# Kernel tuning notes

Measured on AMD Instinct MI355X. Metric: run time of the kernel, lower is better.

The kernel has to match this reference:

```python
import jax, jax.numpy as jnp
import numpy as np

B, C, W = 8, 128, 4096
REDUCTION = 8
D = C // REDUCTION  # 16


def setup_inputs() -> dict:
    key = jax.random.key(0)
    ks = jax.random.split(key, 7)
    scale = 0.05
    return {
        "x": jax.random.normal(ks[0], (B, C, W), dtype=jnp.float32),
        "Wq": jax.random.normal(ks[1], (D, C), dtype=jnp.float32) * scale,
        "bq": jax.random.normal(ks[2], (D,), dtype=jnp.float32) * scale,
        "Wk": jax.random.normal(ks[3], (D, C), dtype=jnp.float32) * scale,
        "bk": jax.random.normal(ks[4], (D,), dtype=jnp.float32) * scale,
        "Wv": jax.random.normal(ks[5], (C, C), dtype=jnp.float32) * scale,
        "bv": jax.random.normal(ks[6], (C,), dtype=jnp.float32) * scale,
    }


def reference(x, Wq, bq, Wk, bk, Wv, bv):
    # 1x1 Conv1d == per-position linear over channel axis
    q = jnp.einsum('dc,bcw->bdw', Wq, x) + bq[None, :, None]   # [B, D, W]
    k = jnp.einsum('dc,bcw->bdw', Wk, x) + bk[None, :, None]   # [B, D, W]
    v = jnp.einsum('oc,bcw->bow', Wv, x) + bv[None, :, None]   # [B, C, W]
    scale = D ** (-0.5)
    # scores[b,i,j] = q[b,:,i] . k[b,:,j]
    scores = jnp.einsum('bdi,bdj->bij', q, k) * scale          # [B, W, W]
    attn = jax.nn.softmax(scores, axis=-1)
    # torch.bmm(value, attn): context[b,c,w] = sum_j v[b,c,j] * attn[b,j,w]
    context = jnp.einsum('bcj,bjw->bcw', v, attn)              # [B, C, W]
    return context + x
```

## Files before the change

kernel.cpp:

```cpp
#include <hip/hip_runtime.h>

#define B_ 8
#define C_ 128
#define W_ 4096
#define D_ 16
#define SCALE2 0.3606737602222409f

typedef short bf16x8 __attribute__((ext_vector_type(8)));
typedef float f32x4 __attribute__((ext_vector_type(4)));
typedef float f32x16 __attribute__((ext_vector_type(16)));

__device__ __forceinline__ unsigned short f2bf(float f) {
    unsigned int u = __float_as_uint(f);
    u += 0x7fffu + ((u >> 16) & 1u);
    return (unsigned short)(u >> 16);
}
__device__ __forceinline__ float bf2f(unsigned short h) {
    return __uint_as_float(((unsigned int)h) << 16);
}
__device__ __forceinline__ unsigned int pk2bf(float lo, float hi) {
    return __builtin_amdgcn_perm(__float_as_uint(hi), __float_as_uint(lo), 0x07060302u);
}
__device__ __forceinline__ bf16x8 u4_to_bf8(unsigned int a, unsigned int b,
                                            unsigned int c, unsigned int d) {
    union { uint4 u; bf16x8 v; } t;
    t.u = make_uint4(a, b, c, d);
    return t.v;
}
__device__ __forceinline__ bf16x8 uint4_as_bf8(uint4 u) {
    union { uint4 u; bf16x8 v; } t;
    t.u = u;
    return t.v;
}
__device__ __forceinline__ uint4 exp2pkq(f32x16 s, int r0) {
    return make_uint4(
        pk2bf(__builtin_amdgcn_exp2f(s[r0+0]), __builtin_amdgcn_exp2f(s[r0+1])),
        pk2bf(__builtin_amdgcn_exp2f(s[r0+2]), __builtin_amdgcn_exp2f(s[r0+3])),
        pk2bf(__builtin_amdgcn_exp2f(s[r0+4]), __builtin_amdgcn_exp2f(s[r0+5])),
        pk2bf(__builtin_amdgcn_exp2f(s[r0+6]), __builtin_amdgcn_exp2f(s[r0+7])));
}
__device__ __forceinline__ int xswz(int j, int c8) {
    return c8 ^ (j & 7) ^ ((j >> 3) & 7);
}

__global__ __launch_bounds__(256) void prep(
    const float* __restrict__ Wq, const float* __restrict__ Wk, const float* __restrict__ Wv,
    unsigned short* __restrict__ Wvbf, unsigned short* __restrict__ Wqkbf)
{
    int g = blockIdx.x * 256 + threadIdx.x;
    const float* src; unsigned short* dst; float sc = 1.0f;
    if (g < 4096)      { src = Wv + g * 4;            dst = Wvbf + g * 4; }
    else if (g < 4608) { int t = g - 4096; src = Wq + t * 4; dst = Wqkbf + t * 4; sc = SCALE2; }
    else               { int t = g - 4608; src = Wk + t * 4; dst = Wqkbf + 2048 + t * 4; }
    float4 v = *(const float4*)src;
    unsigned short h[4] = {f2bf(v.x * sc), f2bf(v.y * sc), f2bf(v.z * sc), f2bf(v.w * sc)};
    *(ushort4*)dst = *(ushort4*)h;
}

__global__ __launch_bounds__(256) void proj(
    const float* __restrict__ x, const unsigned short* __restrict__ Wvbf,
    const unsigned short* __restrict__ Wqkbf,
    const float* __restrict__ bqp, const float* __restrict__ bkp, const float* __restrict__ bvp,
    unsigned short* __restrict__ qws2, unsigned short* __restrict__ kws2,
    unsigned short* __restrict__ vws2)
{
    __shared__ unsigned short xbf[32 * 128];
    __shared__ unsigned short outs[128 * 36];
    __shared__ unsigned short qk_s[2][32][24];

    int b  = blockIdx.x & 7;
    int j0 = (blockIdx.x >> 3) * 32;
    int jt = j0 >> 5;
    int tid = threadIdx.x;
    int wid = tid >> 6, lane = tid & 63, n = lane & 15, q4 = lane >> 4;

    {
        unsigned int* xbf32 = (unsigned int*)xbf;
#pragma unroll
        for (int i = 0; i < 8; i++) {
            int p = tid + 256 * i;
            int c2 = p >> 5;
            int j  = p & 31;
            const float* xp = x + (size_t)(b * C_ + 2 * c2) * W_ + j0 + j;
            float lo = xp[0];
            float hi = xp[W_];
            xbf32[j * 64 + xswz(j, c2 >> 2) * 4 + (c2 & 3)] = pk2bf(lo, hi);
        }
    }
    __syncthreads();

    const f32x4 zero = {0.f, 0.f, 0.f, 0.f};
    f32x4 accv[2][2]; f32x4 accqk = zero;
#pragma unroll
    for (int os = 0; os < 2; os++)
#pragma unroll
        for (int js = 0; js < 2; js++) accv[os][js] = zero;

    int isK = wid >> 1;
    int jsm = wid & 1;

#pragma unroll
    for (int kk = 0; kk < 128; kk += 32) {
        bf16x8 av[2], aqkf, bx[2];
#pragma unroll
        for (int os = 0; os < 2; os++)
            av[os] = *(const bf16x8*)(Wvbf + (wid * 32 + os * 16 + n) * 128 + kk + q4 * 8);
        aqkf = *(const bf16x8*)(Wqkbf + (isK * 16 + n) * 128 + kk + q4 * 8);
#pragma unroll
        for (int js = 0; js < 2; js++) {
            int j = js * 16 + n;
            bx[js] = *(const bf16x8*)&xbf[j * 128 + xswz(j, (kk >> 3) + q4) * 8];
        }
#pragma unroll
        for (int os = 0; os < 2; os++)
#pragma unroll
            for (int js = 0; js < 2; js++)
                accv[os][js] = __builtin_amdgcn_mfma_f32_16x16x32_bf16(av[os], bx[js], accv[os][js], 0, 0, 0);
        accqk = __builtin_amdgcn_mfma_f32_16x16x32_bf16(aqkf, bx[jsm], accqk, 0, 0, 0);
    }

    {
        int pos = jsm * 16 + n;
        const float* bias = isK ? bkp : bqp;
        float bsc = isK ? 1.0f : SCALE2;
#pragma unroll
        for (int r = 0; r < 4; r++)
            qk_s[isK][pos][q4 * 4 + r] = f2bf(accqk[r] + bias[q4 * 4 + r] * bsc);
    }

    float bvv[2][4];
#pragma unroll
    for (int os = 0; os < 2; os++)
#pragma unroll
        for (int r = 0; r < 4; r++) bvv[os][r] = bvp[wid * 32 + os * 16 + q4 * 4 + r];
#pragma unroll
    for (int os = 0; os < 2; os++)
#pragma unroll
        for (int js = 0; js < 2; js++)
#pragma unroll
            for (int r = 0; r < 4; r++) {
                int c = wid * 32 + os * 16 + q4 * 4 + r;
                int j = js * 16 + n;
                outs[c * 36 + j] = f2bf(accv[os][js][r] + bvv[os][r]);
            }
    __syncthreads();

    if (tid < 128) {
        int qk = tid >> 6, hh = (tid >> 5) & 1, jl = tid & 31;
        uint4 v = *(const uint4*)&qk_s[qk][jl][hh * 8];
        unsigned short* dst = (qk ? kws2 : qws2)
            + (size_t)(b * 128 + jt) * 512 + hh * 256 + jl * 8;
        *(uint4*)dst = v;
    }
#pragma unroll
    for (int rep = 0; rep < 2; rep++) {
        int t = tid + rep * 256;
        int c = t & 127, sel = t >> 7;
        int jb = (sel >> 1) * 16 + (sel & 1) * 4;
        uint2 lo = *(const uint2*)&outs[c * 36 + jb];
        uint2 hi = *(const uint2*)&outs[c * 36 + jb + 8];
        *(uint4*)(vws2 + ((size_t)(b * 128 + jt) * 4 + sel) * 1024 + c * 8) =
            make_uint4(lo.x, lo.y, hi.x, hi.y);
    }
}

__global__ __launch_bounds__(256) void row_stats(
    const unsigned short* __restrict__ qws2, const unsigned short* __restrict__ kws2,
    float* __restrict__ rlp)
{
    int blk = blockIdx.x;
    int b = blk & 7;
    int j0 = ((blk >> 3) & 31) * 128;
    int wsp = blk >> 8;
    int tid = threadIdx.x;
    int wid = tid >> 6, lane = tid & 63, wl = lane & 31, h = lane >> 5;

    const unsigned short* qb = qws2 + (size_t)b * 65536;
    const unsigned short* kb = kws2 + (size_t)b * 65536;
    int jt = (j0 >> 5) + wid;

    bf16x8 aq = *(const bf16x8*)(qb + (size_t)jt * 512 + h * 256 + wl * 8);
    f32x16 zero16 = {0.f,0.f,0.f,0.f,0.f,0.f,0.f,0.f,0.f,0.f,0.f,0.f,0.f,0.f,0.f,0.f};

    float lt[16];
#pragma unroll
    for (int r = 0; r < 16; r++) lt[r] = 0.f;

    bf16x8 bkc = *(const bf16x8*)(kb + (size_t)(wsp * 32) * 512 + h * 256 + wl * 8);
    for (int t = 0; t < 32; t++) {
        f32x16 s = __builtin_amdgcn_mfma_f32_32x32x16_bf16(aq, bkc, zero16, 0, 0, 0);
        int tn = wsp * 32 + ((t + 1) & 31);
        bkc = *(const bf16x8*)(kb + (size_t)tn * 512 + h * 256 + wl * 8);
#pragma unroll
        for (int r = 0; r < 16; r++) lt[r] += __builtin_amdgcn_exp2f(s[r]);
    }
#pragma unroll
    for (int mask = 1; mask < 32; mask <<= 1)
#pragma unroll
        for (int r = 0; r < 16; r++) lt[r] += __shfl_xor(lt[r], mask, 64);
    if (wl == 0) {
#pragma unroll
        for (int g = 0; g < 4; g++) {
            f32x4 v = {lt[4*g+0], lt[4*g+1], lt[4*g+2], lt[4*g+3]};
            *(f32x4*)(rlp + (size_t)wsp * 32768 + (size_t)b * W_ + j0 + wid * 32 + 4 * h + 8 * g) = v;
        }
    }
}

__global__ __launch_bounds__(256) void finl(const float* __restrict__ rlp,
                                            float* __restrict__ rls)
{
    int g = blockIdx.x * 256 + threadIdx.x;
    float l = rlp[g] + rlp[32768 + g] + rlp[65536 + g] + rlp[98304 + g];
    rls[g] = 1.0f / l;
}

__global__ __launch_bounds__(256) void vscale(unsigned short* __restrict__ vws2,
                                              const float* __restrict__ rls)
{
    int g = blockIdx.x * 256 + threadIdx.x;
    int hh = (g >> 7) & 1, kf = (g >> 8) & 1, jt = (g >> 9) & 127, b = g >> 16;
    int jb = jt * 32 + kf * 16 + 4 * hh;
    const float* rp = rls + (size_t)b * W_ + jb;
    float4 r0 = *(const float4*)rp;
    float4 r1 = *(const float4*)(rp + 8);
    uint4 v = *(const uint4*)(vws2 + (size_t)g * 8);
    unsigned int o0 = pk2bf(bf2f((unsigned short)(v.x & 0xffffu)) * r0.x,
                            bf2f((unsigned short)(v.x >> 16))     * r0.y);
    unsigned int o1 = pk2bf(bf2f((unsigned short)(v.y & 0xffffu)) * r0.z,
                            bf2f((unsigned short)(v.y >> 16))     * r0.w);
    unsigned int o2 = pk2bf(bf2f((unsigned short)(v.z & 0xffffu)) * r1.x,
                            bf2f((unsigned short)(v.z >> 16))     * r1.y);
    unsigned int o3 = pk2bf(bf2f((unsigned short)(v.w & 0xffffu)) * r1.z,
                            bf2f((unsigned short)(v.w >> 16))     * r1.w);
    *(uint4*)(vws2 + (size_t)g * 8) = make_uint4(o0, o1, o2, o3);
}

__global__ __launch_bounds__(512, 4) void attn_out(
    const float* __restrict__ x, const unsigned short* __restrict__ qws2,
    const unsigned short* __restrict__ kws2, const unsigned short* __restrict__ vws2,
    float* __restrict__ out)
{
    __shared__ uint4 p_lds[2][1024];
    __shared__ float red[128 * 68];

    int b  = blockIdx.x & 7;
    int w0 = (blockIdx.x >> 3) * 64;
    int tid = threadIdx.x;
    int wid = tid >> 6, lane = tid & 63, wl = lane & 31, h = lane >> 5;
    int cq = wid >> 1, kh = wid & 1;

    const unsigned short* qb  = qws2 + (size_t)b * 65536;
    const unsigned short* kb  = kws2 + (size_t)b * 65536;
    const uint4* vtb4 = (const uint4*)(vws2 + (size_t)b * 524288) + h * 128 + (cq * 32 + wl);
    const int qoff = h * 256 + wl * 8;

    bf16x8 bk = *(const bf16x8*)(kb + (size_t)((w0 >> 5) + kh) * 512 + h * 256 + wl * 8);

    f32x16 zero16 = {0.f,0.f,0.f,0.f,0.f,0.f,0.f,0.f,0.f,0.f,0.f,0.f,0.f,0.f,0.f,0.f};
    f32x16 acc[2];
    acc[0] = zero16; acc[1] = zero16;

    const int wbase = cq * 256 + h * 64 + kh * 32 + wl;
    const int rbase = kh * 512 + h * 64 + wl;

    bf16x8 aq = *(const bf16x8*)(qb + (size_t)cq * 512 + qoff);
    uint4 vf[4];
#pragma unroll
    for (int kf = 0; kf < 4; kf++)
        vf[kf] = vtb4[(size_t)(kh * 4 + kf) * 256];
    {
        f32x16 s = __builtin_amdgcn_mfma_f32_32x32x16_bf16(aq, bk, zero16, 0, 0, 0);
        aq = *(const bf16x8*)(qb + (size_t)(4 + cq) * 512 + qoff);
        p_lds[0][wbase]       = exp2pkq(s, 0);
        p_lds[0][wbase + 128] = exp2pkq(s, 8);
    }
    __syncthreads();

#pragma unroll 2
    for (int it = 0; it < 32; it++) {
        int cur = it & 1, nxt = cur ^ 1;
        uint4 vfn[4];
#pragma unroll
        for (int kf = 0; kf < 4; kf++) {
            int kg = ((it + 1) & 31) * 8 + kh * 4 + kf;
            vfn[kf] = vtb4[(size_t)kg * 256];
        }
        f32x16 s = __builtin_amdgcn_mfma_f32_32x32x16_bf16(aq, bk, zero16, 0, 0, 0);
        aq = *(const bf16x8*)(qb + (size_t)(((it + 2) & 31) * 4 + cq) * 512 + qoff);
        p_lds[nxt][wbase]       = exp2pkq(s, 0);
        p_lds[nxt][wbase + 128] = exp2pkq(s, 8);
        __builtin_amdgcn_s_setprio(1);
#pragma unroll
        for (int kf = 0; kf < 4; kf++) {
            bf16x8 af = uint4_as_bf8(vf[kf]);
#pragma unroll
            for (int nt = 0; nt < 2; nt++) {
                bf16x8 bp = uint4_as_bf8(p_lds[cur][rbase + kf * 128 + nt * 32]);
                acc[nt] = __builtin_amdgcn_mfma_f32_32x32x16_bf16(af, bp, acc[nt], 0, 0, 0);
            }
        }
        __builtin_amdgcn_s_setprio(0);
        __syncthreads();
#pragma unroll
        for (int kf = 0; kf < 4; kf++) vf[kf] = vfn[kf];
    }

#define CROW(r) (cq * 32 + ((r) & 3) + 8 * ((r) >> 2) + 4 * h)
    if (kh == 1) {
#pragma unroll
        for (int nt = 0; nt < 2; nt++)
#pragma unroll
            for (int r = 0; r < 16; r++)
                red[CROW(r) * 68 + nt * 32 + wl] = acc[nt][r];
    }
    __syncthreads();
    if (kh == 0) {
#pragma unroll
        for (int nt = 0; nt < 2; nt++)
#pragma unroll
            for (int r = 0; r < 16; r++) {
                int o = CROW(r) * 68 + nt * 32 + wl;
                red[o] += acc[nt][r];
            }
    }
#undef CROW
    __syncthreads();

#pragma unroll
    for (int u = 0; u < 4; u++) {
        int k = tid + 512 * u;
        int c = k >> 4, wseg = (k & 15) * 4;
        size_t gidx = (size_t)(b * C_ + c) * W_ + w0 + wseg;
        float4 xv = *(const float4*)(x + gidx);
        const float* sp = &red[c * 68 + wseg];
        *(float4*)(out + gidx) = make_float4(sp[0] + xv.x, sp[1] + xv.y, sp[2] + xv.z, sp[3] + xv.w);
    }
}

extern "C" void kernel_launch(void* const* d_in, const int* in_sizes, int n_in,
                              void* d_out, int out_size, void* d_ws, size_t ws_size,
                              hipStream_t stream)
{
    const float* x  = (const float*)d_in[0];
    const float* Wq = (const float*)d_in[1];
    const float* bq = (const float*)d_in[2];
    const float* Wk = (const float*)d_in[3];
    const float* bk = (const float*)d_in[4];
    const float* Wv = (const float*)d_in[5];
    const float* bv = (const float*)d_in[6];
    float* out = (float*)d_out;

    unsigned short* qws2 = (unsigned short*)d_ws;
    unsigned short* kws2 = qws2 + (size_t)524288;
    unsigned short* vws2 = kws2 + (size_t)524288;
    unsigned short* Wvbf = vws2 + (size_t)4194304;
    unsigned short* Wqkbf = Wvbf + 16384;
    float* rlp = (float*)(Wqkbf + 4096);
    float* rls = rlp + 131072;

    prep<<<20, 256, 0, stream>>>(Wq, Wk, Wv, Wvbf, Wqkbf);
    proj<<<1024, 256, 0, stream>>>(x, Wvbf, Wqkbf, bq, bk, bv, qws2, kws2, vws2);
    row_stats<<<1024, 256, 0, stream>>>(qws2, kws2, rlp);
    finl<<<128, 256, 0, stream>>>(rlp, rls);
    vscale<<<2048, 256, 0, stream>>>(vws2, rls);
    attn_out<<<512, 512, 0, stream>>>(x, qws2, kws2, vws2, out);
}
```

Before: 158.3 us.

## Fold softmax normalization into exponent and drop separate V-scaling kernel

The value-scaling pass over the whole bf16 V workspace is removed, along with the reciprocal kernel. The finalize kernel now writes log2 of each column's softmax denominator, and attn_out subtracts it inside exp2, so P already carries the normalization. The main loop is also hand-unrolled with explicit A/B register buffers for the V fragments, and the exp2/LDS store is moved after the PV MFMAs. This saves a full read and write of V plus one launch, at the cost of extra per-iteration loads of the log terms and one subtract per exp inside the hot loop.

```diff
diff --git a/kernel.cpp b/kernel.cpp
--- a/kernel.cpp
+++ b/kernel.cpp
@@ -21,23 +21,17 @@
 __device__ __forceinline__ unsigned int pk2bf(float lo, float hi) {
     return __builtin_amdgcn_perm(__float_as_uint(hi), __float_as_uint(lo), 0x07060302u);
 }
-__device__ __forceinline__ bf16x8 u4_to_bf8(unsigned int a, unsigned int b,
-                                            unsigned int c, unsigned int d) {
-    union { uint4 u; bf16x8 v; } t;
-    t.u = make_uint4(a, b, c, d);
-    return t.v;
-}
 __device__ __forceinline__ bf16x8 uint4_as_bf8(uint4 u) {
     union { uint4 u; bf16x8 v; } t;
     t.u = u;
     return t.v;
 }
-__device__ __forceinline__ uint4 exp2pkq(f32x16 s, int r0) {
+__device__ __forceinline__ uint4 exp2s(f32x16 s, int r0, float4 ra, float4 rb) {
     return make_uint4(
-        pk2bf(__builtin_amdgcn_exp2f(s[r0+0]), __builtin_amdgcn_exp2f(s[r0+1])),
-        pk2bf(__builtin_amdgcn_exp2f(s[r0+2]), __builtin_amdgcn_exp2f(s[r0+3])),
-        pk2bf(__builtin_amdgcn_exp2f(s[r0+4]), __builtin_amdgcn_exp2f(s[r0+5])),
-        pk2bf(__builtin_amdgcn_exp2f(s[r0+6]), __builtin_amdgcn_exp2f(s[r0+7])));
+        pk2bf(__builtin_amdgcn_exp2f(s[r0+0]-ra.x), __builtin_amdgcn_exp2f(s[r0+1]-ra.y)),
+        pk2bf(__builtin_amdgcn_exp2f(s[r0+2]-ra.z), __builtin_amdgcn_exp2f(s[r0+3]-ra.w)),
+        pk2bf(__builtin_amdgcn_exp2f(s[r0+4]-rb.x), __builtin_amdgcn_exp2f(s[r0+5]-rb.y)),
+        pk2bf(__builtin_amdgcn_exp2f(s[r0+6]-rb.z), __builtin_amdgcn_exp2f(s[r0+7]-rb.w)));
 }
 __device__ __forceinline__ int xswz(int j, int c8) {
     return c8 ^ (j & 7) ^ ((j >> 3) & 7);
@@ -207,39 +201,18 @@
     }
 }
 
-__global__ __launch_bounds__(256) void finl(const float* __restrict__ rlp,
-                                            float* __restrict__ rls)
+__global__ __launch_bounds__(256) void rfin(const float* __restrict__ rlp,
+                                            float* __restrict__ rlog)
 {
     int g = blockIdx.x * 256 + threadIdx.x;
     float l = rlp[g] + rlp[32768 + g] + rlp[65536 + g] + rlp[98304 + g];
-    rls[g] = 1.0f / l;
-}
-
-__global__ __launch_bounds__(256) void vscale(unsigned short* __restrict__ vws2,
-                                              const float* __restrict__ rls)
-{
-    int g = blockIdx.x * 256 + threadIdx.x;
-    int hh = (g >> 7) & 1, kf = (g >> 8) & 1, jt = (g >> 9) & 127, b = g >> 16;
-    int jb = jt * 32 + kf * 16 + 4 * hh;
-    const float* rp = rls + (size_t)b * W_ + jb;
-    float4 r0 = *(const float4*)rp;
-    float4 r1 = *(const float4*)(rp + 8);
-    uint4 v = *(const uint4*)(vws2 + (size_t)g * 8);
-    unsigned int o0 = pk2bf(bf2f((unsigned short)(v.x & 0xffffu)) * r0.x,
-                            bf2f((unsigned short)(v.x >> 16))     * r0.y);
-    unsigned int o1 = pk2bf(bf2f((unsigned short)(v.y & 0xffffu)) * r0.z,
-                            bf2f((unsigned short)(v.y >> 16))     * r0.w);
-    unsigned int o2 = pk2bf(bf2f((unsigned short)(v.z & 0xffffu)) * r1.x,
-                            bf2f((unsigned short)(v.z >> 16))     * r1.y);
-    unsigned int o3 = pk2bf(bf2f((unsigned short)(v.w & 0xffffu)) * r1.z,
-                            bf2f((unsigned short)(v.w >> 16))     * r1.w);
-    *(uint4*)(vws2 + (size_t)g * 8) = make_uint4(o0, o1, o2, o3);
+    rlog[g] = __builtin_amdgcn_logf(l);
 }
 
 __global__ __launch_bounds__(512, 4) void attn_out(
     const float* __restrict__ x, const unsigned short* __restrict__ qws2,
     const unsigned short* __restrict__ kws2, const unsigned short* __restrict__ vws2,
-    float* __restrict__ out)
+    const float* __restrict__ rlog, float* __restrict__ out)
 {
     __shared__ uint4 p_lds[2][1024];
     __shared__ float red[128 * 68];
@@ -253,6 +226,7 @@
     const unsigned short* qb  = qws2 + (size_t)b * 65536;
     const unsigned short* kb  = kws2 + (size_t)b * 65536;
     const uint4* vtb4 = (const uint4*)(vws2 + (size_t)b * 524288) + h * 128 + (cq * 32 + wl);
+    const float* rlb = rlog + (size_t)b * W_;
     const int qoff = h * 256 + wl * 8;
 
     bf16x8 bk = *(const bf16x8*)(kb + (size_t)((w0 >> 5) + kh) * 512 + h * 256 + wl * 8);
@@ -265,46 +239,55 @@
     const int rbase = kh * 512 + h * 64 + wl;
 
     bf16x8 aq = *(const bf16x8*)(qb + (size_t)cq * 512 + qoff);
-    uint4 vf[4];
+    uint4 vfA[4], vfB[4];
 #pragma unroll
     for (int kf = 0; kf < 4; kf++)
-        vf[kf] = vtb4[(size_t)(kh * 4 + kf) * 256];
+        vfA[kf] = vtb4[(size_t)(kh * 4 + kf) * 256];
     {
+        int jb0 = cq * 32 + 4 * h;
+        float4 rl0 = *(const float4*)(rlb + jb0);
+        float4 rl1 = *(const float4*)(rlb + jb0 + 8);
+        float4 rl2 = *(const float4*)(rlb + jb0 + 16);
+        float4 rl3 = *(const float4*)(rlb + jb0 + 24);
         f32x16 s = __builtin_amdgcn_mfma_f32_32x32x16_bf16(aq, bk, zero16, 0, 0, 0);
         aq = *(const bf16x8*)(qb + (size_t)(4 + cq) * 512 + qoff);
-        p_lds[0][wbase]       = exp2pkq(s, 0);
-        p_lds[0][wbase + 128] = exp2pkq(s, 8);
-    }
-    __syncthreads();
-
-#pragma unroll 2
-    for (int it = 0; it < 32; it++) {
-        int cur = it & 1, nxt = cur ^ 1;
-        uint4 vfn[4];
-#pragma unroll
-        for (int kf = 0; kf < 4; kf++) {
-            int kg = ((it + 1) & 31) * 8 + kh * 4 + kf;
-            vfn[kf] = vtb4[(size_t)kg * 256];
-        }
-        f32x16 s = __builtin_amdgcn_mfma_f32_32x32x16_bf16(aq, bk, zero16, 0, 0, 0);
-        aq = *(const bf16x8*)(qb + (size_t)(((it + 2) & 31) * 4 + cq) * 512 + qoff);
-        p_lds[nxt][wbase]       = exp2pkq(s, 0);
-        p_lds[nxt][wbase + 128] = exp2pkq(s, 8);
-        __builtin_amdgcn_s_setprio(1);
-#pragma unroll
-        for (int kf = 0; kf < 4; kf++) {
-            bf16x8 af = uint4_as_bf8(vf[kf]);
-#pragma unroll
-            for (int nt = 0; nt < 2; nt++) {
-                bf16x8 bp = uint4_as_bf8(p_lds[cur][rbase + kf * 128 + nt * 32]);
-                acc[nt] = __builtin_amdgcn_mfma_f32_32x32x16_bf16(af, bp, acc[nt], 0, 0, 0);
-            }
-        }
-        __builtin_amdgcn_s_setprio(0);
-        __syncthreads();
-#pragma unroll
-        for (int kf = 0; kf < 4; kf++) vf[kf] = vfn[kf];
-    }
+        p_lds[0][wbase]       = exp2s(s, 0, rl0, rl1);
+        p_lds[0][wbase + 128] = exp2s(s, 8, rl2, rl3);
+    }
+    __syncthreads();
+
+#define STEP(IT, CUR, VC, VN)                                                        \
+    {                                                                                \
+        const int it_ = (IT);                                                        \
+        int kgb = ((it_ + 1) & 31) * 8 + kh * 4;                                     \
+        _Pragma("unroll") for (int kf = 0; kf < 4; kf++)                             \
+            VN[kf] = vtb4[(size_t)(kgb + kf) * 256];                                 \
+        int jbn = ((it_ + 1) & 31) * 128 + cq * 32 + 4 * h;                          \
+        float4 rl0 = *(const float4*)(rlb + jbn);                                    \
+        float4 rl1 = *(const float4*)(rlb + jbn + 8);                                \
+        float4 rl2 = *(const float4*)(rlb + jbn + 16);                               \
+        float4 rl3 = *(const float4*)(rlb + jbn + 24);                               \
+        f32x16 s = __builtin_amdgcn_mfma_f32_32x32x16_bf16(aq, bk, zero16, 0, 0, 0); \
+        aq = *(const bf16x8*)(qb + (size_t)(((it_ + 2) & 31) * 4 + cq) * 512 + qoff);\
+        __builtin_amdgcn_s_setprio(1);                                               \
+        _Pragma("unroll") for (int kf = 0; kf < 4; kf++) {                           \
+            bf16x8 af = uint4_as_bf8(VC[kf]);                                        \
+            _Pragma("unroll") for (int nt = 0; nt < 2; nt++) {                       \
+                bf16x8 bp = uint4_as_bf8(p_lds[CUR][rbase + kf * 128 + nt * 32]);    \
+                acc[nt] = __builtin_amdgcn_mfma_f32_32x32x16_bf16(af, bp, acc[nt], 0, 0, 0); \
+            }                                                                        \
+        }                                                                            \
+        __builtin_amdgcn_s_setprio(0);                                               \
+        p_lds[(CUR) ^ 1][wbase]       = exp2s(s, 0, rl0, rl1);                       \
+        p_lds[(CUR) ^ 1][wbase + 128] = exp2s(s, 8, rl2, rl3);                       \
+        __syncthreads();                                                             \
+    }
+
+    for (int i2 = 0; i2 < 16; i2++) {
+        STEP(2 * i2,     0, vfA, vfB);
+        STEP(2 * i2 + 1, 1, vfB, vfA);
+    }
+#undef STEP
 
 #define CROW(r) (cq * 32 + ((r) & 3) + 8 * ((r) >> 2) + 4 * h)
     if (kh == 1) {
@@ -357,12 +340,11 @@
     unsigned short* Wvbf = vws2 + (size_t)4194304;
     unsigned short* Wqkbf = Wvbf + 16384;
     float* rlp = (float*)(Wqkbf + 4096);
-    float* rls = rlp + 131072;
+    float* rlg = rlp + 131072;
 
     prep<<<20, 256, 0, stream>>>(Wq, Wk, Wv, Wvbf, Wqkbf);
     proj<<<1024, 256, 0, stream>>>(x, Wvbf, Wqkbf, bq, bk, bv, qws2, kws2, vws2);
     row_stats<<<1024, 256, 0, stream>>>(qws2, kws2, rlp);
-    finl<<<128, 256, 0, stream>>>(rlp, rls);
-    vscale<<<2048, 256, 0, stream>>>(vws2, rls);
-    attn_out<<<512, 512, 0, stream>>>(x, qws2, kws2, vws2, out);
-}
+    rfin<<<128, 256, 0, stream>>>(rlp, rlg);
+    attn_out<<<512, 512, 0, stream>>>(x, qws2, kws2, vws2, rlg, out);
+}
```

Result: slower. 163.1 us (+3.1%).

## Split attn_out channels across two blocks and restructure the P pipeline

Applied to the files above, without the earlier changes.

Changes attn_out from 512-thread blocks covering all 128 channels to 256-thread blocks covering 64 channels each, with twice as many blocks. Each block now walks the keys in 64 steps of 32 instead of 32 steps of 64. The loop is manually unrolled by two with ping-pong V registers, and the P exp/store is moved after the PV MFMAs so it overlaps with them. The aim is better occupancy and more blocks to fill the CUs, at the cost of recomputing the QK scores and exponentials twice per position (once per channel half).

```diff
diff --git a/kernel.cpp b/kernel.cpp
--- a/kernel.cpp
+++ b/kernel.cpp
@@ -20,12 +20,6 @@
 }
 __device__ __forceinline__ unsigned int pk2bf(float lo, float hi) {
     return __builtin_amdgcn_perm(__float_as_uint(hi), __float_as_uint(lo), 0x07060302u);
-}
-__device__ __forceinline__ bf16x8 u4_to_bf8(unsigned int a, unsigned int b,
-                                            unsigned int c, unsigned int d) {
-    union { uint4 u; bf16x8 v; } t;
-    t.u = make_uint4(a, b, c, d);
-    return t.v;
 }
 __device__ __forceinline__ bf16x8 uint4_as_bf8(uint4 u) {
     union { uint4 u; bf16x8 v; } t;
@@ -236,75 +230,79 @@
     *(uint4*)(vws2 + (size_t)g * 8) = make_uint4(o0, o1, o2, o3);
 }
 
-__global__ __launch_bounds__(512, 4) void attn_out(
+__global__ __launch_bounds__(256, 4) void attn_out(
     const float* __restrict__ x, const unsigned short* __restrict__ qws2,
     const unsigned short* __restrict__ kws2, const unsigned short* __restrict__ vws2,
     float* __restrict__ out)
 {
-    __shared__ uint4 p_lds[2][1024];
-    __shared__ float red[128 * 68];
-
-    int b  = blockIdx.x & 7;
-    int w0 = (blockIdx.x >> 3) * 64;
+    __shared__ uint4 p_lds[2][512];
+    __shared__ float red[64 * 68];
+
+    int bi = blockIdx.x;
+    int b  = bi & 7;
+    int rem = bi >> 3;
+    int w0 = (rem & 63) * 64;
+    int ch = rem >> 6;
     int tid = threadIdx.x;
     int wid = tid >> 6, lane = tid & 63, wl = lane & 31, h = lane >> 5;
-    int cq = wid >> 1, kh = wid & 1;
-
-    const unsigned short* qb  = qws2 + (size_t)b * 65536;
-    const unsigned short* kb  = kws2 + (size_t)b * 65536;
-    const uint4* vtb4 = (const uint4*)(vws2 + (size_t)b * 524288) + h * 128 + (cq * 32 + wl);
+    int jh = wid >> 1, wh = wid & 1;
+    int cq = wid & 1,  kh = wid >> 1;
+
+    const unsigned short* qb = qws2 + (size_t)b * 65536;
+    const unsigned short* kb = kws2 + (size_t)b * 65536;
+    const uint4* vtb4 = (const uint4*)(vws2 + (size_t)b * 524288)
+                        + h * 128 + (ch * 64 + cq * 32 + wl);
     const int qoff = h * 256 + wl * 8;
 
-    bf16x8 bk = *(const bf16x8*)(kb + (size_t)((w0 >> 5) + kh) * 512 + h * 256 + wl * 8);
+    bf16x8 bk = *(const bf16x8*)(kb + (size_t)((w0 >> 5) + wh) * 512 + h * 256 + wl * 8);
 
     f32x16 zero16 = {0.f,0.f,0.f,0.f,0.f,0.f,0.f,0.f,0.f,0.f,0.f,0.f,0.f,0.f,0.f,0.f};
     f32x16 acc[2];
     acc[0] = zero16; acc[1] = zero16;
 
-    const int wbase = cq * 256 + h * 64 + kh * 32 + wl;
-    const int rbase = kh * 512 + h * 64 + wl;
-
-    bf16x8 aq = *(const bf16x8*)(qb + (size_t)cq * 512 + qoff);
-    uint4 vf[4];
-#pragma unroll
-    for (int kf = 0; kf < 4; kf++)
-        vf[kf] = vtb4[(size_t)(kh * 4 + kf) * 256];
+    const int wbase = (2 * jh) * 128 + h * 64 + wh * 32 + wl;
+    const int rbase = (2 * kh) * 128 + h * 64 + wl;
+
+    bf16x8 aq = *(const bf16x8*)(qb + (size_t)jh * 512 + qoff);
+    uint4 vfA[2], vfB[2];
+#pragma unroll
+    for (int kf = 0; kf < 2; kf++)
+        vfA[kf] = vtb4[(size_t)(kh * 2 + kf) * 256];
     {
         f32x16 s = __builtin_amdgcn_mfma_f32_32x32x16_bf16(aq, bk, zero16, 0, 0, 0);
-        aq = *(const bf16x8*)(qb + (size_t)(4 + cq) * 512 + qoff);
+        aq = *(const bf16x8*)(qb + (size_t)(2 + jh) * 512 + qoff);
         p_lds[0][wbase]       = exp2pkq(s, 0);
         p_lds[0][wbase + 128] = exp2pkq(s, 8);
     }
     __syncthreads();
 
-#pragma unroll 2
-    for (int it = 0; it < 32; it++) {
-        int cur = it & 1, nxt = cur ^ 1;
-        uint4 vfn[4];
-#pragma unroll
-        for (int kf = 0; kf < 4; kf++) {
-            int kg = ((it + 1) & 31) * 8 + kh * 4 + kf;
-            vfn[kf] = vtb4[(size_t)kg * 256];
-        }
-        f32x16 s = __builtin_amdgcn_mfma_f32_32x32x16_bf16(aq, bk, zero16, 0, 0, 0);
-        aq = *(const bf16x8*)(qb + (size_t)(((it + 2) & 31) * 4 + cq) * 512 + qoff);
-        p_lds[nxt][wbase]       = exp2pkq(s, 0);
-        p_lds[nxt][wbase + 128] = exp2pkq(s, 8);
-        __builtin_amdgcn_s_setprio(1);
-#pragma unroll
-        for (int kf = 0; kf < 4; kf++) {
-            bf16x8 af = uint4_as_bf8(vf[kf]);
-#pragma unroll
-            for (int nt = 0; nt < 2; nt++) {
-                bf16x8 bp = uint4_as_bf8(p_lds[cur][rbase + kf * 128 + nt * 32]);
-                acc[nt] = __builtin_amdgcn_mfma_f32_32x32x16_bf16(af, bp, acc[nt], 0, 0, 0);
-            }
-        }
-        __builtin_amdgcn_s_setprio(0);
-        __syncthreads();
-#pragma unroll
-        for (int kf = 0; kf < 4; kf++) vf[kf] = vfn[kf];
-    }
+#define STEP(IT, CUR, VC, VN)                                                        \
+    {                                                                                \
+        const int it_ = (IT);                                                        \
+        int gb = ((it_ + 1) & 63) * 4 + kh * 2;                                      \
+        VN[0] = vtb4[(size_t)(gb + 0) * 256];                                        \
+        VN[1] = vtb4[(size_t)(gb + 1) * 256];                                        \
+        f32x16 s = __builtin_amdgcn_mfma_f32_32x32x16_bf16(aq, bk, zero16, 0, 0, 0); \
+        aq = *(const bf16x8*)(qb + (size_t)(((it_ + 2) & 63) * 2 + jh) * 512 + qoff);\
+        __builtin_amdgcn_s_setprio(1);                                               \
+        _Pragma("unroll") for (int kf = 0; kf < 2; kf++) {                           \
+            bf16x8 af = uint4_as_bf8(VC[kf]);                                        \
+            _Pragma("unroll") for (int nt = 0; nt < 2; nt++) {                       \
+                bf16x8 bp = uint4_as_bf8(p_lds[CUR][rbase + kf * 128 + nt * 32]);    \
+                acc[nt] = __builtin_amdgcn_mfma_f32_32x32x16_bf16(af, bp, acc[nt], 0, 0, 0); \
+            }                                                                        \
+        }                                                                            \
+        __builtin_amdgcn_s_setprio(0);                                               \
+        p_lds[(CUR) ^ 1][wbase]       = exp2pkq(s, 0);                               \
+        p_lds[(CUR) ^ 1][wbase + 128] = exp2pkq(s, 8);                               \
+        __syncthreads();                                                             \
+    }
+
+    for (int i2 = 0; i2 < 32; i2++) {
+        STEP(2 * i2,     0, vfA, vfB);
+        STEP(2 * i2 + 1, 1, vfB, vfA);
+    }
+#undef STEP
 
 #define CROW(r) (cq * 32 + ((r) & 3) + 8 * ((r) >> 2) + 4 * h)
     if (kh == 1) {
@@ -329,11 +327,12 @@
 
 #pragma unroll
     for (int u = 0; u < 4; u++) {
-        int k = tid + 512 * u;
-        int c = k >> 4, wseg = (k & 15) * 4;
+        int k = tid + 256 * u;
+        int cl = k >> 4, wseg = (k & 15) * 4;
+        int c = ch * 64 + cl;
         size_t gidx = (size_t)(b * C_ + c) * W_ + w0 + wseg;
         float4 xv = *(const float4*)(x + gidx);
-        const float* sp = &red[c * 68 + wseg];
+        const float* sp = &red[cl * 68 + wseg];
         *(float4*)(out + gidx) = make_float4(sp[0] + xv.x, sp[1] + xv.y, sp[2] + xv.z, sp[3] + xv.w);
     }
 }
@@ -364,5 +363,5 @@
     row_stats<<<1024, 256, 0, stream>>>(qws2, kws2, rlp);
     finl<<<128, 256, 0, stream>>>(rlp, rls);
     vscale<<<2048, 256, 0, stream>>>(vws2, rls);
-    attn_out<<<512, 512, 0, stream>>>(x, qws2, kws2, vws2, out);
-}
+    attn_out<<<1024, 256, 0, stream>>>(x, qws2, kws2, vws2, out);
+}
```

Measured after the change: 164.8 us. 4.2% more time.
